# Performance work log

Measured on AMD Instinct MI355X. Metric: run time of the kernel, lower is better.

The kernel has to match this reference:

```python
import jax, jax.numpy as jnp
import numpy as np

B, N, C, H = 8, 4096, 768, 8
EPS = 1e-12  # F.normalize eps


def setup_inputs() -> dict:
    key = jax.random.key(0)
    ks = jax.random.split(key, 4)
    x = jax.random.normal(ks[0], (B, N, C), dtype=jnp.float32)
    w_qkv = jax.random.normal(ks[1], (3 * C, C), dtype=jnp.float32) * 0.02
    temperature = jnp.ones((H, 1, 1), dtype=jnp.float32)
    w_proj = jax.random.normal(ks[2], (C, C), dtype=jnp.float32) * 0.02
    b_proj = jnp.zeros((C,), dtype=jnp.float32)
    return {"x": x, "w_qkv": w_qkv, "temperature": temperature,
            "w_proj": w_proj, "b_proj": b_proj}


def _l2norm(t):
    # F.normalize(t, dim=-1): t / max(||t||_2, eps)
    n = jnp.sqrt(jnp.sum(t * t, axis=-1, keepdims=True))
    return t / jnp.maximum(n, EPS)


def reference(x, w_qkv, temperature, w_proj, b_proj):
    b, n, c = x.shape
    h = H
    hd = c // h
    # qkv projection: (B,N,3C) -> (3,B,H,hd,N)
    qkv = (x @ w_qkv.T).reshape(b, n, 3, h, hd)
    qkv = jnp.transpose(qkv, (2, 0, 3, 4, 1))
    q, k, v = qkv[0], qkv[1], qkv[2]          # each (B,H,hd,N)
    qn = _l2norm(q)                            # normalize over N (token) dim
    kn = _l2norm(k)
    # small per-head covariance attention: (B,H,hd,hd)
    attn = jnp.einsum('bhdn,bhen->bhde', qn, kn) * temperature
    attn = jax.nn.softmax(attn, axis=-1)
    out = jnp.einsum('bhde,bhen->bhdn', attn, v)  # (B,H,hd,N)
    out = jnp.transpose(out, (0, 3, 1, 2)).reshape(b, n, c)
    return out @ w_proj.T + b_proj
```

## Files before the change

kernel.cpp:

```cpp
#include <hip/hip_runtime.h>
#include <cstdint>
#include <cstddef>

#define B_ 8
#define N_ 4096
#define C_ 768
#define H_ 8
#define HD_ 96
#define EPSN 1e-12f
#define NS_ 4

typedef short s16x8 __attribute__((ext_vector_type(8)));
typedef short s16x4 __attribute__((ext_vector_type(4)));
typedef float f32x4 __attribute__((ext_vector_type(4)));

static __device__ __forceinline__ short f2bf(float f) {
  unsigned u = __float_as_uint(f);
  unsigned r = (u + 0x7fff + ((u >> 16) & 1)) >> 16;
  return (short)r;
}
static __device__ __forceinline__ float bf2f(unsigned short s) {
  return __uint_as_float(((unsigned)s) << 16);
}
static __device__ __forceinline__ s16x8 pack8(const float4 a, const float4 b) {
  s16x8 r;
  r[0] = f2bf(a.x); r[1] = f2bf(a.y); r[2] = f2bf(a.z); r[3] = f2bf(a.w);
  r[4] = f2bf(b.x); r[5] = f2bf(b.y); r[6] = f2bf(b.z); r[7] = f2bf(b.w);
  return r;
}

#define TSW(ch, t) ((t) ^ ((((ch) >> 2) & 7) << 3))

static __device__ __forceinline__ int swz(int s) {
  return s ^ (((s >> 7) & 3) << 3);
}

static __device__ __forceinline__ void gld16(const short* g, short* l) {
  __builtin_amdgcn_global_load_lds(
      (const __attribute__((address_space(1))) void*)g,
      (__attribute__((address_space(3))) void*)l, 16, 0, 0);
}

__global__ __launch_bounds__(256)
void xcvt(const float* __restrict__ x, short* __restrict__ xb) {
  const int n8 = (B_ * N_ * C_) / 8;
  for (int i = blockIdx.x * 256 + threadIdx.x; i < n8; i += gridDim.x * 256) {
    const float4 a = *(const float4*)(x + (size_t)i * 8);
    const float4 b = *(const float4*)(x + (size_t)i * 8 + 4);
    *(s16x8*)(xb + (size_t)i * 8) = pack8(a, b);
  }
}

__global__ __launch_bounds__(256)
void wcvt(const float* __restrict__ w, short* __restrict__ wb) {
  const int i = blockIdx.x * 256 + threadIdx.x;
  const float4 a = *(const float4*)(w + (size_t)i * 8);
  const float4 b = *(const float4*)(w + (size_t)i * 8 + 4);
  *(s16x8*)(wb + (size_t)i * 8) = pack8(a, b);
}

template<int BF>
__global__ __launch_bounds__(256)
void gram_p(const float* __restrict__ x, const short* __restrict__ xb,
            float* __restrict__ Gp) {
  const int f = blockIdx.x;
  const int xcd = f & 7;
  const int t = f >> 3;
  const int pair = t % 21;
  const int cdiv = t / 21;
  const int c = xcd + 8 * cdiv;
  const int split = c & 3;
  const int b = c >> 2;

  int rem = pair, ti = 0;
#pragma unroll
  for (int it = 0; it < 5; ++it)
    if (rem >= 6 - ti) { rem -= 6 - ti; ++ti; }
  const int tj = ti + rem;
  const int i0 = ti * 128, j0 = tj * 128;
  const bool diag = (ti == tj);

  const int tid = threadIdx.x;
  const int lane = tid & 63, wave = tid >> 6;
  const int l15 = lane & 15, quad = lane >> 4;
  const int wm = wave & 1, wn = wave >> 1;

  __shared__ __align__(16) short smem[2 * 128 * 72];
  short* At = smem;
  short* Bt = smem + 128 * 72;

  const int tg = tid >> 4;
  const int cg = tid & 15;
  const int t0 = tg * 4;
  const int c0 = cg * 4;
  const float* xbF = x + (size_t)b * N_ * C_;
  const short* xbB = xb + (size_t)b * N_ * C_;

  f32x4 acc[4][4] = {};

  const int nbeg = split * (N_ / NS_);
  const int nend = nbeg + (N_ / NS_);
  for (int n0 = nbeg; n0 < nend; n0 += 64) {
    if (BF) {
      s16x8 la[4], lb[4];
#pragma unroll
      for (int r = 0; r < 4; ++r)
        la[r] = *(const s16x8*)(xbB + (size_t)(n0 + t0 + r) * C_ + i0 + cg * 8);
      if (!diag) {
#pragma unroll
        for (int r = 0; r < 4; ++r)
          lb[r] = *(const s16x8*)(xbB + (size_t)(n0 + t0 + r) * C_ + j0 + cg * 8);
      }
      __syncthreads();
#pragma unroll
      for (int cc = 0; cc < 8; ++cc) {
        const int ch = cg * 8 + cc;
        s16x4 v;
        v[0] = la[0][cc]; v[1] = la[1][cc]; v[2] = la[2][cc]; v[3] = la[3][cc];
        *(s16x4*)&At[ch * 72 + TSW(ch, t0)] = v;
      }
      if (!diag) {
#pragma unroll
        for (int cc = 0; cc < 8; ++cc) {
          const int ch = cg * 8 + cc;
          s16x4 v;
          v[0] = lb[0][cc]; v[1] = lb[1][cc]; v[2] = lb[2][cc]; v[3] = lb[3][cc];
          *(s16x4*)&Bt[ch * 72 + TSW(ch, t0)] = v;
        }
      }
      __syncthreads();
    } else {
      float4 la[2][4], lb[2][4];
#pragma unroll
      for (int q = 0; q < 2; ++q)
#pragma unroll
        for (int r = 0; r < 4; ++r)
          la[q][r] = *(const float4*)(xbF + (size_t)(n0 + t0 + r) * C_ + i0 + c0 + q * 64);
      if (!diag) {
#pragma unroll
        for (int q = 0; q < 2; ++q)
#pragma unroll
          for (int r = 0; r < 4; ++r)
            lb[q][r] = *(const float4*)(xbF + (size_t)(n0 + t0 + r) * C_ + j0 + c0 + q * 64);
      }
      __syncthreads();
#pragma unroll
      for (int q = 0; q < 2; ++q)
#pragma unroll
        for (int cc = 0; cc < 4; ++cc) {
          const int ch = c0 + q * 64 + cc;
          s16x4 v;
          v[0] = f2bf(((const float*)&la[q][0])[cc]);
          v[1] = f2bf(((const float*)&la[q][1])[cc]);
          v[2] = f2bf(((const float*)&la[q][2])[cc]);
          v[3] = f2bf(((const float*)&la[q][3])[cc]);
          *(s16x4*)&At[ch * 72 + TSW(ch, t0)] = v;
        }
      if (!diag) {
#pragma unroll
        for (int q = 0; q < 2; ++q)
#pragma unroll
          for (int cc = 0; cc < 4; ++cc) {
            const int ch = c0 + q * 64 + cc;
            s16x4 v;
            v[0] = f2bf(((const float*)&lb[q][0])[cc]);
            v[1] = f2bf(((const float*)&lb[q][1])[cc]);
            v[2] = f2bf(((const float*)&lb[q][2])[cc]);
            v[3] = f2bf(((const float*)&lb[q][3])[cc]);
            *(s16x4*)&Bt[ch * 72 + TSW(ch, t0)] = v;
          }
      }
      __syncthreads();
    }
    const short* Bre = diag ? At : Bt;
#pragma unroll
    for (int ks = 0; ks < 64; ks += 32) {
      s16x8 af[4], bfr[4];
#pragma unroll
      for (int mi = 0; mi < 4; ++mi) {
        const int ch = wm * 64 + mi * 16 + l15;
        af[mi] = *(const s16x8*)&At[ch * 72 + TSW(ch, ks + quad * 8)];
      }
#pragma unroll
      for (int ni = 0; ni < 4; ++ni) {
        const int ch = wn * 64 + ni * 16 + l15;
        bfr[ni] = *(const s16x8*)&Bre[ch * 72 + TSW(ch, ks + quad * 8)];
      }
#pragma unroll
      for (int ni = 0; ni < 4; ++ni)
#pragma unroll
        for (int mi = 0; mi < 4; ++mi)
          acc[mi][ni] = __builtin_amdgcn_mfma_f32_16x16x32_bf16(af[mi], bfr[ni], acc[mi][ni], 0, 0, 0);
    }
  }

  float* Gpb = Gp + (((size_t)b * 21 + pair) * NS_ + split) * (128 * 128);
#pragma unroll
  for (int mi = 0; mi < 4; ++mi)
#pragma unroll
    for (int ni = 0; ni < 4; ++ni) {
      const int ii = wm * 64 + mi * 16 + quad * 4;
      const int jj = wn * 64 + ni * 16 + l15;
#pragma unroll
      for (int r = 0; r < 4; ++r)
        Gpb[(ii + r) * 128 + jj] = acc[mi][ni][r];
    }
}

__global__ __launch_bounds__(256)
void gram_red(const float* __restrict__ Gp, short* __restrict__ G) {
  const int pair = blockIdx.x;
  int rem = pair, ti = 0;
#pragma unroll
  for (int it = 0; it < 5; ++it)
    if (rem >= 6 - ti) { rem -= 6 - ti; ++ti; }
  const int tj = ti + rem;
  const int b = blockIdx.y;
  const int i0 = ti * 128, j0 = tj * 128;
  const bool diag = (ti == tj);
  const int tid = threadIdx.x;

  __shared__ short Ts[128 * 137];

  const float4* P = (const float4*)(Gp + (((size_t)b * 21 + pair) * NS_) * (128 * 128));
  short* Gb = G + (size_t)b * C_ * C_;

#pragma unroll
  for (int it = 0; it < 16; ++it) {
    const int q = tid + it * 256;
    const int row = q >> 5;
    const int c4 = q & 31;
    float4 v = P[q];
    const float4 v1 = P[q + 4096];
    const float4 v2 = P[q + 8192];
    const float4 v3 = P[q + 12288];
    v.x += v1.x + v2.x + v3.x;
    v.y += v1.y + v2.y + v3.y;
    v.z += v1.z + v2.z + v3.z;
    v.w += v1.w + v2.w + v3.w;
    s16x4 sv;
    sv[0] = f2bf(v.x); sv[1] = f2bf(v.y); sv[2] = f2bf(v.z); sv[3] = f2bf(v.w);
    *(s16x4*)&Gb[(size_t)(i0 + row) * C_ + j0 + c4 * 4] = sv;
    if (!diag) {
#pragma unroll
      for (int c = 0; c < 4; ++c)
        Ts[(c4 * 4 + c) * 137 + row] = sv[c];
    }
  }
  if (!diag) {
    __syncthreads();
#pragma unroll
    for (int p = 0; p < 8; ++p) {
      const int id = tid + p * 256;
      const int j = id >> 4, cs = (id & 15) * 8;
      *(s16x8*)&Gb[(size_t)(j0 + j) * C_ + i0 + cs] = *(const s16x8*)&Ts[j * 137 + cs];
    }
  }
}

__global__ __launch_bounds__(256)
void gemm_nt_bf(const short* __restrict__ A, const short* __restrict__ Bb,
                short* __restrict__ Out, size_t sB, size_t sO) {
  const int z = blockIdx.z;
  const int n0 = blockIdx.x * 128;
  const int m0 = blockIdx.y * 128;
  const int tid = threadIdx.x;
  const int lane = tid & 63, wave = tid >> 6;
  const int l15 = lane & 15, quad = lane >> 4;
  const int wm = wave & 1, wn = wave >> 1;

  __shared__ __align__(16) short As[2][128 * 32];
  __shared__ __align__(16) short Bs[2][128 * 32];

  const short* asrc[2]; const short* bsrc[2];
  int doff[2];
#pragma unroll
  for (int cc = 0; cc < 2; ++cc) {
    const int P = wave * 1024 + cc * 512 + lane * 8;
    const int L = swz(P);
    const int row = L >> 5, col = L & 31;
    asrc[cc] = A + (size_t)(m0 + row) * C_ + col;
    bsrc[cc] = Bb + (size_t)z * sB + (size_t)(n0 + row) * C_ + col;
    doff[cc] = wave * 1024 + cc * 512;
  }

  f32x4 acc[4][4] = {};

#pragma unroll
  for (int cc = 0; cc < 2; ++cc) {
    gld16(asrc[cc], &As[0][doff[cc]]);
    gld16(bsrc[cc], &Bs[0][doff[cc]]);
  }
  __syncthreads();
  int cur = 0;
  for (int k0 = 0; k0 < C_; k0 += 32) {
    const int nx = k0 + 32;
    if (nx < C_) {
#pragma unroll
      for (int cc = 0; cc < 2; ++cc) {
        gld16(asrc[cc] + nx, &As[cur ^ 1][doff[cc]]);
        gld16(bsrc[cc] + nx, &Bs[cur ^ 1][doff[cc]]);
      }
    }
    s16x8 af[4];
#pragma unroll
    for (int mi = 0; mi < 4; ++mi)
      af[mi] = *(const s16x8*)&As[cur][swz((wm * 64 + mi * 16 + l15) * 32 + quad * 8)];
#pragma unroll
    for (int ni = 0; ni < 4; ++ni) {
      const s16x8 bf = *(const s16x8*)&Bs[cur][swz((wn * 64 + ni * 16 + l15) * 32 + quad * 8)];
#pragma unroll
      for (int mi = 0; mi < 4; ++mi)
        acc[mi][ni] = __builtin_amdgcn_mfma_f32_16x16x32_bf16(af[mi], bf, acc[mi][ni], 0, 0, 0);
    }
    __syncthreads();
    cur ^= 1;
  }

  short* ob = Out + (size_t)z * sO;
#pragma unroll
  for (int mi = 0; mi < 4; ++mi) {
    const int m = m0 + wm * 64 + mi * 16 + quad * 4;
#pragma unroll
    for (int ni = 0; ni < 4; ++ni) {
      const int n = n0 + wn * 64 + ni * 16 + l15;
#pragma unroll
      for (int r = 0; r < 4; ++r)
        ob[(size_t)(m + r) * C_ + n] = f2bf(acc[mi][ni][r]);
    }
  }
}

__global__ __launch_bounds__(256)
void gemm_fb(const float* __restrict__ A, const short* __restrict__ Bb,
             short* __restrict__ Out, size_t sB, size_t sO) {
  const int z = blockIdx.z;
  const int n0 = blockIdx.x * 128;
  const int m0 = blockIdx.y * 128;
  const int tid = threadIdx.x;
  const int lane = tid & 63, wave = tid >> 6;
  const int l15 = lane & 15, quad = lane >> 4;
  const int wm = wave & 1, wn = wave >> 1;

  __shared__ __align__(16) short As[2][128 * 40];
  __shared__ __align__(16) short Bs[2][128 * 32];

  const int ar = tid >> 1;
  const int ak = (tid & 1) * 16;
  const float* ap = A + (size_t)(m0 + ar) * C_ + ak;

  const short* bsrc[2];
  int doff[2];
#pragma unroll
  for (int cc = 0; cc < 2; ++cc) {
    const int P = wave * 1024 + cc * 512 + lane * 8;
    const int L = swz(P);
    bsrc[cc] = Bb + (size_t)z * sB + (size_t)(n0 + (L >> 5)) * C_ + (L & 31);
    doff[cc] = wave * 1024 + cc * 512;
  }

  f32x4 acc[4][4] = {};

  {
    const float4 a0 = *(const float4*)(ap + 0);
    const float4 a1 = *(const float4*)(ap + 4);
    const float4 a2 = *(const float4*)(ap + 8);
    const float4 a3 = *(const float4*)(ap + 12);
#pragma unroll
    for (int cc = 0; cc < 2; ++cc) gld16(bsrc[cc], &Bs[0][doff[cc]]);
    *(s16x8*)&As[0][ar * 40 + ak]     = pack8(a0, a1);
    *(s16x8*)&As[0][ar * 40 + ak + 8] = pack8(a2, a3);
  }
  __syncthreads();
  int cur = 0;
  for (int k0 = 0; k0 < C_; k0 += 32) {
    const int nx = k0 + 32;
    float4 a0, a1, a2, a3;
    if (nx < C_) {
      a0 = *(const float4*)(ap + nx + 0);
      a1 = *(const float4*)(ap + nx + 4);
      a2 = *(const float4*)(ap + nx + 8);
      a3 = *(const float4*)(ap + nx + 12);
#pragma unroll
      for (int cc = 0; cc < 2; ++cc) gld16(bsrc[cc] + nx, &Bs[cur ^ 1][doff[cc]]);
    }
    s16x8 af[4];
#pragma unroll
    for (int mi = 0; mi < 4; ++mi)
      af[mi] = *(const s16x8*)&As[cur][(wm * 64 + mi * 16 + l15) * 40 + quad * 8];
#pragma unroll
    for (int ni = 0; ni < 4; ++ni) {
      const s16x8 bf = *(const s16x8*)&Bs[cur][swz((wn * 64 + ni * 16 + l15) * 32 + quad * 8)];
#pragma unroll
      for (int mi = 0; mi < 4; ++mi)
        acc[mi][ni] = __builtin_amdgcn_mfma_f32_16x16x32_bf16(af[mi], bf, acc[mi][ni], 0, 0, 0);
    }
    if (nx < C_) {
      *(s16x8*)&As[cur ^ 1][ar * 40 + ak]     = pack8(a0, a1);
      *(s16x8*)&As[cur ^ 1][ar * 40 + ak + 8] = pack8(a2, a3);
    }
    __syncthreads();
    cur ^= 1;
  }

  short* ob = Out + (size_t)z * sO;
#pragma unroll
  for (int mi = 0; mi < 4; ++mi) {
    const int m = m0 + wm * 64 + mi * 16 + quad * 4;
#pragma unroll
    for (int ni = 0; ni < 4; ++ni) {
      const int n = n0 + wn * 64 + ni * 16 + l15;
#pragma unroll
      for (int r = 0; r < 4; ++r)
        ob[(size_t)(m + r) * C_ + n] = f2bf(acc[mi][ni][r]);
    }
  }
}

__global__ __launch_bounds__(256)
void row_norms(const short* __restrict__ Y, const float* __restrict__ w_qkv,
               float* __restrict__ norms) {
  const int b = blockIdx.y;
  const int m = blockIdx.x * 4 + (threadIdx.x >> 6);
  const int lane = threadIdx.x & 63;
  const short* y = Y + ((size_t)b * 1536 + m) * C_;
  const float* w = w_qkv + (size_t)m * C_;
  float s = 0.f;
#pragma unroll
  for (int j = 0; j < 3; ++j) {
    const int o = j * 256 + lane * 4;
    const s16x4 yv = *(const s16x4*)(y + o);
    const float4 wv = *(const float4*)(w + o);
    s += bf2f((unsigned short)yv[0]) * wv.x + bf2f((unsigned short)yv[1]) * wv.y +
         bf2f((unsigned short)yv[2]) * wv.z + bf2f((unsigned short)yv[3]) * wv.w;
  }
#pragma unroll
  for (int o = 32; o > 0; o >>= 1) s += __shfl_xor(s, o);
  if (lane == 0) {
    int idx;
    if (m < 768) idx = (b * 8 + m / 96) * 96 + (m % 96);
    else { const int mm = m - 768; idx = B_ * H_ * 96 + (b * 8 + mm / 96) * 96 + (mm % 96); }
    norms[idx] = s;
  }
}

__global__ __launch_bounds__(512)
void s_attn(const short* __restrict__ Y, const short* __restrict__ wb,
            const float* __restrict__ norms, const float* __restrict__ temp,
            float* __restrict__ S) {
  const int bh = blockIdx.x;
  const int b = bh >> 3, h = bh & 7;
  const int tid = threadIdx.x;
  const int lane = tid & 63, wave = tid >> 6;
  const int l15 = lane & 15, quad = lane >> 4;

  __shared__ __align__(16) float Sf[96 * 97];
  __shared__ float qsc[96], ksc[96];
  short* Ys = (short*)Sf;
  short* Ks = (short*)Sf + 96 * 72;

  if (tid < 96)
    qsc[tid] = temp[h] / fmaxf(sqrtf(norms[bh * 96 + tid]), EPSN);
  else if (tid < 192)
    ksc[tid - 96] = 1.0f / fmaxf(sqrtf(norms[B_ * H_ * 96 + bh * 96 + (tid - 96)]), EPSN);

  const short* yb = Y + ((size_t)b * 1536 + h * 96) * C_;
  const short* kb = wb + (size_t)(768 + h * 96) * C_;

  int dts[5], ets[5];
#pragma unroll
  for (int j = 0; j < 5; ++j) {
    const int t = j * 8 + wave;
    dts[j] = t / 6; ets[j] = t % 6;
  }

  f32x4 sc[5] = {};
  const int r0 = tid >> 3, c80 = (tid & 7) * 8;
  const int id1 = tid + 512;
  const int r1 = id1 >> 3, c81 = (id1 & 7) * 8;
  for (int k0 = 0; k0 < C_; k0 += 64) {
    s16x8 yv0, kv0, yv1, kv1;
    yv0 = *(const s16x8*)(yb + (size_t)r0 * C_ + k0 + c80);
    kv0 = *(const s16x8*)(kb + (size_t)r0 * C_ + k0 + c80);
    if (tid < 256) {
      yv1 = *(const s16x8*)(yb + (size_t)r1 * C_ + k0 + c81);
      kv1 = *(const s16x8*)(kb + (size_t)r1 * C_ + k0 + c81);
    }
    __syncthreads();
    *(s16x8*)&Ys[r0 * 72 + c80] = yv0;
    *(s16x8*)&Ks[r0 * 72 + c80] = kv0;
    if (tid < 256) {
      *(s16x8*)&Ys[r1 * 72 + c81] = yv1;
      *(s16x8*)&Ks[r1 * 72 + c81] = kv1;
    }
    __syncthreads();
#pragma unroll
    for (int j = 0; j < 5; ++j) {
      const int t = j * 8 + wave;
      if (t < 36) {
#pragma unroll
        for (int kk = 0; kk < 64; kk += 32) {
          const s16x8 a  = *(const s16x8*)&Ys[(dts[j] * 16 + l15) * 72 + kk + quad * 8];
          const s16x8 bb = *(const s16x8*)&Ks[(ets[j] * 16 + l15) * 72 + kk + quad * 8];
          sc[j] = __builtin_amdgcn_mfma_f32_16x16x32_bf16(a, bb, sc[j], 0, 0, 0);
        }
      }
    }
  }
  __syncthreads();
#pragma unroll
  for (int j = 0; j < 5; ++j) {
    const int t = j * 8 + wave;
    if (t < 36) {
      const int e = ets[j] * 16 + l15;
      const float kf = ksc[e];
#pragma unroll
      for (int r = 0; r < 4; ++r) {
        const int d = dts[j] * 16 + quad * 4 + r;
        Sf[d * 97 + e] = sc[j][r] * qsc[d] * kf;
      }
    }
  }
  __syncthreads();
  float* Sb = S + (size_t)bh * (HD_ * HD_);
  for (int rr = 0; rr < 12; ++rr) {
    const int d = wave * 12 + rr;
    const float v0 = Sf[d * 97 + lane];
    const float v1 = (lane < 32) ? Sf[d * 97 + 64 + lane] : -1e30f;
    float mx = fmaxf(v0, v1);
#pragma unroll
    for (int o = 32; o > 0; o >>= 1) mx = fmaxf(mx, __shfl_xor(mx, o));
    const float e0 = __expf(v0 - mx);
    const float e1 = (lane < 32) ? __expf(v1 - mx) : 0.0f;
    float sum = e0 + e1;
#pragma unroll
    for (int o = 32; o > 0; o >>= 1) sum += __shfl_xor(sum, o);
    const float inv = 1.0f / sum;
    Sb[d * 96 + lane] = e0 * inv;
    if (lane < 32) Sb[d * 96 + 64 + lane] = e1 * inv;
  }
}

__global__ __launch_bounds__(256)
void av_gemm(const float* __restrict__ S, const float* __restrict__ w_qkv,
             short* __restrict__ AVt) {
  const int bh = blockIdx.x;
  const int b = bh >> 3, h = bh & 7;
  const int ct = blockIdx.y * 64;
  const int tid = threadIdx.x;
  __shared__ float at[96 * 97];
  __shared__ float wv[96 * 64];
  const float* Sb = S + (size_t)bh * (HD_ * HD_);
  for (int i = tid; i < 96 * 96; i += 256)
    at[(i / 96) * 97 + (i % 96)] = Sb[i];
  for (int i = tid; i < 96 * 64; i += 256) {
    const int e = i >> 6, c = i & 63;
    wv[e * 64 + c] = w_qkv[(size_t)(2 * C_ + h * 96 + e) * C_ + ct + c];
  }
  __syncthreads();
  const int d0 = (tid >> 4) * 6;
  const int c0 = (tid & 15) * 4;
  float acc[6][4] = {};
  for (int e = 0; e < 96; ++e) {
    const float4 bv = *(const float4*)&wv[e * 64 + c0];
    float aa[6];
#pragma unroll
    for (int i = 0; i < 6; ++i) aa[i] = at[(d0 + i) * 97 + e];
#pragma unroll
    for (int i = 0; i < 6; ++i) {
      acc[i][0] += aa[i] * bv.x; acc[i][1] += aa[i] * bv.y;
      acc[i][2] += aa[i] * bv.z; acc[i][3] += aa[i] * bv.w;
    }
  }
  short* AVb = AVt + (size_t)b * C_ * C_;
#pragma unroll
  for (int i = 0; i < 6; ++i)
#pragma unroll
    for (int j = 0; j < 4; ++j)
      AVb[(size_t)(ct + c0 + j) * C_ + h * 96 + d0 + i] = f2bf(acc[i][j]);
}

__global__ __launch_bounds__(256)
void gemm_xm_bf(const short* __restrict__ xb, const short* __restrict__ Mb,
                const float* __restrict__ bias, float* __restrict__ out) {
  const int f = blockIdx.x;
  const int xcd = f & 7;
  const int t = f >> 3;
  const int j6 = t % 6;
  const int sdiv = t / 6;
  const int s = xcd + 8 * sdiv;
  const int z = s >> 5;
  const int n0 = j6 * 128;
  const int m0 = (s & 31) * 128;
  const int tid = threadIdx.x;
  const int lane = tid & 63;
  const int wave = tid >> 6;
  const int l15 = lane & 15;
  const int quad = lane >> 4;
  const int wm = wave & 1;
  const int wn = wave >> 1;

  __shared__ __align__(16) short As[2][128 * 32];
  __shared__ __align__(16) short Bs[2][128 * 32];

  const short* asrc[2]; const short* bsrc[2];
  int doff[2];
#pragma unroll
  for (int cc = 0; cc < 2; ++cc) {
    const int P = wave * 1024 + cc * 512 + lane * 8;
    const int L = swz(P);
    const int row = L >> 5, col = L & 31;
    asrc[cc] = xb + ((size_t)z * N_ + m0 + row) * C_ + col;
    bsrc[cc] = Mb + (size_t)z * C_ * C_ + (size_t)(n0 + row) * C_ + col;
    doff[cc] = wave * 1024 + cc * 512;
  }

  f32x4 acc[4][4] = {};

#pragma unroll
  for (int cc = 0; cc < 2; ++cc) {
    gld16(asrc[cc], &As[0][doff[cc]]);
    gld16(bsrc[cc], &Bs[0][doff[cc]]);
  }
  __syncthreads();
  int cur = 0;
  for (int k0 = 0; k0 < C_; k0 += 32) {
    const int nx = k0 + 32;
    if (nx < C_) {
#pragma unroll
      for (int cc = 0; cc < 2; ++cc) {
        gld16(asrc[cc] + nx, &As[cur ^ 1][doff[cc]]);
        gld16(bsrc[cc] + nx, &Bs[cur ^ 1][doff[cc]]);
      }
    }
    s16x8 af[4];
#pragma unroll
    for (int mi = 0; mi < 4; ++mi)
      af[mi] = *(const s16x8*)&As[cur][swz((wm * 64 + mi * 16 + l15) * 32 + quad * 8)];
#pragma unroll
    for (int ni = 0; ni < 4; ++ni) {
      const s16x8 bf = *(const s16x8*)&Bs[cur][swz((wn * 64 + ni * 16 + l15) * 32 + quad * 8)];
#pragma unroll
      for (int mi = 0; mi < 4; ++mi)
        acc[mi][ni] = __builtin_amdgcn_mfma_f32_16x16x32_bf16(af[mi], bf, acc[mi][ni], 0, 0, 0);
    }
    __syncthreads();
    cur ^= 1;
  }

  float bv[4];
#pragma unroll
  for (int ni = 0; ni < 4; ++ni) bv[ni] = bias[n0 + wn * 64 + ni * 16 + l15];
#pragma unroll
  for (int mi = 0; mi < 4; ++mi) {
    const int m = m0 + wm * 64 + mi * 16 + quad * 4;
#pragma unroll
    for (int ni = 0; ni < 4; ++ni) {
      const int n = n0 + wn * 64 + ni * 16 + l15;
      float* dst = out + ((size_t)z * N_ + m) * C_ + n;
#pragma unroll
      for (int r = 0; r < 4; ++r)
        dst[(size_t)r * C_] = acc[mi][ni][r] + bv[ni];
    }
  }
}

__global__ __launch_bounds__(256)
void gemm_xm_f32(const float* __restrict__ x, const short* __restrict__ Mb,
                 const float* __restrict__ bias, float* __restrict__ out) {
  const int f = blockIdx.x;
  const int xcd = f & 7;
  const int t = f >> 3;
  const int j6 = t % 6;
  const int sdiv = t / 6;
  const int s = xcd + 8 * sdiv;
  const int z = s >> 5;
  const int n0 = j6 * 128;
  const int m0 = (s & 31) * 128;
  const int tid = threadIdx.x;
  const int lane = tid & 63;
  const int wave = tid >> 6;
  const int l15 = lane & 15;
  const int quad = lane >> 4;
  const int wm = wave & 1;
  const int wn = wave >> 1;

  __shared__ __align__(16) short As[128 * 40];
  __shared__ __align__(16) short Bs[128 * 40];

  const int ar = tid >> 1;
  const int ak = (tid & 1) * 16;
  const float* xp = x + ((size_t)z * N_ + m0 + ar) * C_ + ak;
  const short* mp = Mb + (size_t)z * C_ * C_ + (size_t)(n0 + ar) * C_ + ak;

  f32x4 acc[4][4] = {};

  for (int k0 = 0; k0 < C_; k0 += 32) {
    const float4 a0 = *(const float4*)(xp + k0 + 0);
    const float4 a1 = *(const float4*)(xp + k0 + 4);
    const float4 a2 = *(const float4*)(xp + k0 + 8);
    const float4 a3 = *(const float4*)(xp + k0 + 12);
    const s16x8 b0 = *(const s16x8*)(mp + k0 + 0);
    const s16x8 b1 = *(const s16x8*)(mp + k0 + 8);
    __syncthreads();
    *(s16x8*)&As[ar * 40 + ak]     = pack8(a0, a1);
    *(s16x8*)&As[ar * 40 + ak + 8] = pack8(a2, a3);
    *(s16x8*)&Bs[ar * 40 + ak]     = b0;
    *(s16x8*)&Bs[ar * 40 + ak + 8] = b1;
    __syncthreads();
    s16x8 af[4];
#pragma unroll
    for (int mi = 0; mi < 4; ++mi)
      af[mi] = *(const s16x8*)&As[(wm * 64 + mi * 16 + l15) * 40 + quad * 8];
#pragma unroll
    for (int ni = 0; ni < 4; ++ni) {
      const s16x8 bf = *(const s16x8*)&Bs[(wn * 64 + ni * 16 + l15) * 40 + quad * 8];
#pragma unroll
      for (int mi = 0; mi < 4; ++mi)
        acc[mi][ni] = __builtin_amdgcn_mfma_f32_16x16x32_bf16(af[mi], bf, acc[mi][ni], 0, 0, 0);
    }
  }

  float bv[4];
#pragma unroll
  for (int ni = 0; ni < 4; ++ni) bv[ni] = bias[n0 + wn * 64 + ni * 16 + l15];
#pragma unroll
  for (int mi = 0; mi < 4; ++mi) {
    const int m = m0 + wm * 64 + mi * 16 + quad * 4;
#pragma unroll
    for (int ni = 0; ni < 4; ++ni) {
      const int n = n0 + wn * 64 + ni * 16 + l15;
      float* dst = out + ((size_t)z * N_ + m) * C_ + n;
#pragma unroll
      for (int r = 0; r < 4; ++r)
        dst[(size_t)r * C_] = acc[mi][ni][r] + bv[ni];
    }
  }
}

extern "C" void kernel_launch(void* const* d_in, const int* in_sizes, int n_in,
                              void* d_out, int out_size, void* d_ws, size_t ws_size,
                              hipStream_t stream) {
  const float* x      = (const float*)d_in[0];
  const float* w_qkv  = (const float*)d_in[1];
  const float* temp   = (const float*)d_in[2];
  const float* w_proj = (const float*)d_in[3];
  const float* b_proj = (const float*)d_in[4];
  float* out = (float*)d_out;

  char* base = (char*)d_ws;
  float* S     = (float*)base;
  float* norms = (float*)(base + 2359296);
  short* G     = (short*)(base + 2408448);
  short* AVt   = G;
  short* Mb    = (short*)(base + 11845632);
  short* Y     = (short*)(base + 21282816);
  short* wb    = (short*)(base + 11845632);

  const size_t need1 = 55885824 + 50331648;
  const size_t need2 = 40157184 + 50331648;
  const int tier = (ws_size >= need1) ? 1 : (ws_size >= need2) ? 2 : 3;

  float* Gp = (tier == 2) ? (float*)(base + 40157184) : (float*)(base + 11845632);
  short* xb = (tier == 1) ? (short*)(base + 55885824)
            : (tier == 2) ? (short*)(base + 40157184) : nullptr;

  if (tier == 1) {
    xcvt<<<3072, 256, 0, stream>>>(x, xb);
    gram_p<1><<<21 * NS_ * B_, 256, 0, stream>>>(x, xb, Gp);
  } else {
    gram_p<0><<<21 * NS_ * B_, 256, 0, stream>>>(x, xb ? xb : (const short*)G, Gp);
  }

  gram_red<<<dim3(21, B_), 256, 0, stream>>>(Gp, G);

  if (tier == 2) xcvt<<<3072, 256, 0, stream>>>(x, xb);

  wcvt<<<576, 256, 0, stream>>>(w_qkv, wb);

  gemm_nt_bf<<<dim3(C_ / 128, 1536 / 128, B_), 256, 0, stream>>>(
      wb, G, Y, (size_t)C_ * C_, (size_t)1536 * C_);

  row_norms<<<dim3(1536 / 4, B_), 256, 0, stream>>>(Y, w_qkv, norms);

  s_attn<<<B_ * H_, 512, 0, stream>>>(Y, wb, norms, temp, S);

  av_gemm<<<dim3(B_ * H_, C_ / 64), 256, 0, stream>>>(S, w_qkv, AVt);

  gemm_fb<<<dim3(C_ / 128, C_ / 128, B_), 256, 0, stream>>>(
      w_proj, AVt, Mb, (size_t)C_ * C_, (size_t)C_ * C_);

  if (tier == 3)
    gemm_xm_f32<<<C_ / 128 * (N_ / 128) * B_, 256, 0, stream>>>(x, Mb, b_proj, out);
  else
    gemm_xm_bf<<<C_ / 128 * (N_ / 128) * B_, 256, 0, stream>>>(xb, Mb, b_proj, out);
}
```

Before: 399.1 us.

## Deepen GEMM prefetch to two tiles with explicit vmcnt waits and setprio

Both bf16 GEMM kernels now issue loads for the first two K-tiles up front and prefetch tile t+2 after each compute step. A partial s_waitcnt vmcnt(4) lets the next tile's loads stay in flight instead of draining the whole queue, and raw s_barrier with sched_barrier fences keeps the compiler from reordering around it. The MFMA section runs at raised wave priority via s_setprio. Correctness now depends on the hand-counted vmcnt matching how many loads gld16 issues per tile.

```diff
diff --git a/kernel.cpp b/kernel.cpp
--- a/kernel.cpp
+++ b/kernel.cpp
@@ -291,21 +291,24 @@
     gld16(asrc[cc], &As[0][doff[cc]]);
     gld16(bsrc[cc], &Bs[0][doff[cc]]);
   }
-  __syncthreads();
+#pragma unroll
+  for (int cc = 0; cc < 2; ++cc) {
+    gld16(asrc[cc] + 32, &As[1][doff[cc]]);
+    gld16(bsrc[cc] + 32, &Bs[1][doff[cc]]);
+  }
+
   int cur = 0;
-  for (int k0 = 0; k0 < C_; k0 += 32) {
-    const int nx = k0 + 32;
-    if (nx < C_) {
-#pragma unroll
-      for (int cc = 0; cc < 2; ++cc) {
-        gld16(asrc[cc] + nx, &As[cur ^ 1][doff[cc]]);
-        gld16(bsrc[cc] + nx, &Bs[cur ^ 1][doff[cc]]);
-      }
-    }
+  const int NT = C_ / 32;
+  for (int t = 0; t < NT; ++t) {
+    if (t < NT - 1) asm volatile("s_waitcnt vmcnt(4)" ::: "memory");
+    else            asm volatile("s_waitcnt vmcnt(0)" ::: "memory");
+    __builtin_amdgcn_sched_barrier(0);
+    __builtin_amdgcn_s_barrier();
     s16x8 af[4];
 #pragma unroll
     for (int mi = 0; mi < 4; ++mi)
       af[mi] = *(const s16x8*)&As[cur][swz((wm * 64 + mi * 16 + l15) * 32 + quad * 8)];
+    __builtin_amdgcn_s_setprio(1);
 #pragma unroll
     for (int ni = 0; ni < 4; ++ni) {
       const s16x8 bf = *(const s16x8*)&Bs[cur][swz((wn * 64 + ni * 16 + l15) * 32 + quad * 8)];
@@ -313,7 +316,18 @@
       for (int mi = 0; mi < 4; ++mi)
         acc[mi][ni] = __builtin_amdgcn_mfma_f32_16x16x32_bf16(af[mi], bf, acc[mi][ni], 0, 0, 0);
     }
-    __syncthreads();
+    __builtin_amdgcn_s_setprio(0);
+    __builtin_amdgcn_sched_barrier(0);
+    __builtin_amdgcn_s_barrier();
+    __builtin_amdgcn_sched_barrier(0);
+    if (t + 2 < NT) {
+      const int nx = (t + 2) * 32;
+#pragma unroll
+      for (int cc = 0; cc < 2; ++cc) {
+        gld16(asrc[cc] + nx, &As[cur][doff[cc]]);
+        gld16(bsrc[cc] + nx, &Bs[cur][doff[cc]]);
+      }
+    }
     cur ^= 1;
   }
 
@@ -585,9 +599,9 @@
                 const float* __restrict__ bias, float* __restrict__ out) {
   const int f = blockIdx.x;
   const int xcd = f & 7;
-  const int t = f >> 3;
-  const int j6 = t % 6;
-  const int sdiv = t / 6;
+  const int t6 = f >> 3;
+  const int j6 = t6 % 6;
+  const int sdiv = t6 / 6;
   const int s = xcd + 8 * sdiv;
   const int z = s >> 5;
   const int n0 = j6 * 128;
@@ -622,21 +636,24 @@
     gld16(asrc[cc], &As[0][doff[cc]]);
     gld16(bsrc[cc], &Bs[0][doff[cc]]);
   }
-  __syncthreads();
+#pragma unroll
+  for (int cc = 0; cc < 2; ++cc) {
+    gld16(asrc[cc] + 32, &As[1][doff[cc]]);
+    gld16(bsrc[cc] + 32, &Bs[1][doff[cc]]);
+  }
+
   int cur = 0;
-  for (int k0 = 0; k0 < C_; k0 += 32) {
-    const int nx = k0 + 32;
-    if (nx < C_) {
-#pragma unroll
-      for (int cc = 0; cc < 2; ++cc) {
-        gld16(asrc[cc] + nx, &As[cur ^ 1][doff[cc]]);
-        gld16(bsrc[cc] + nx, &Bs[cur ^ 1][doff[cc]]);
-      }
-    }
+  const int NT = C_ / 32;
+  for (int t = 0; t < NT; ++t) {
+    if (t < NT - 1) asm volatile("s_waitcnt vmcnt(4)" ::: "memory");
+    else            asm volatile("s_waitcnt vmcnt(0)" ::: "memory");
+    __builtin_amdgcn_sched_barrier(0);
+    __builtin_amdgcn_s_barrier();
     s16x8 af[4];
 #pragma unroll
     for (int mi = 0; mi < 4; ++mi)
       af[mi] = *(const s16x8*)&As[cur][swz((wm * 64 + mi * 16 + l15) * 32 + quad * 8)];
+    __builtin_amdgcn_s_setprio(1);
 #pragma unroll
     for (int ni = 0; ni < 4; ++ni) {
       const s16x8 bf = *(const s16x8*)&Bs[cur][swz((wn * 64 + ni * 16 + l15) * 32 + quad * 8)];
@@ -644,7 +661,18 @@
       for (int mi = 0; mi < 4; ++mi)
         acc[mi][ni] = __builtin_amdgcn_mfma_f32_16x16x32_bf16(af[mi], bf, acc[mi][ni], 0, 0, 0);
     }
-    __syncthreads();
+    __builtin_amdgcn_s_setprio(0);
+    __builtin_amdgcn_sched_barrier(0);
+    __builtin_amdgcn_s_barrier();
+    __builtin_amdgcn_sched_barrier(0);
+    if (t + 2 < NT) {
+      const int nx = (t + 2) * 32;
+#pragma unroll
+      for (int cc = 0; cc < 2; ++cc) {
+        gld16(asrc[cc] + nx, &As[cur][doff[cc]]);
+        gld16(bsrc[cc] + nx, &Bs[cur][doff[cc]]);
+      }
+    }
     cur ^= 1;
   }
 
```

Result: no change. 399.0 us (-0.0%).
